# Kernel optimization log

Hardware: AMD Instinct MI355X
Metric: run time of the kernel (lower is better)

## Reference

```python
import jax, jax.numpy as jnp
import numpy as np

V, E, H = 32000, 512, 512
B, S = 64, 128

def setup_inputs() -> dict:
    key = jax.random.key(0)
    ks = jax.random.split(key, 8)
    scale = 1.0 / np.sqrt(H)
    return {
        "decoder_input": jax.random.randint(ks[0], (B, S), 0, V),
        "encoder_hidden": jax.random.normal(ks[1], (1, B, H), dtype=jnp.float32),
        "encoder_output": jax.random.normal(ks[2], (B, S, H), dtype=jnp.float32),
        "emb_table": jax.random.normal(ks[3], (V, E), dtype=jnp.float32),
        "W_ih": jax.random.uniform(ks[4], (3 * H, E), dtype=jnp.float32, minval=-scale, maxval=scale),
        "W_hh": jax.random.uniform(ks[5], (3 * H, H), dtype=jnp.float32, minval=-scale, maxval=scale),
        "b_ih": jax.random.uniform(ks[6], (3 * H,), dtype=jnp.float32, minval=-scale, maxval=scale),
        "b_hh": jax.random.uniform(ks[7], (3 * H,), dtype=jnp.float32, minval=-scale, maxval=scale),
        "epoch": 0,
    }

def _gru_cell(x, h, W_ih, W_hh, b_ih, b_hh):
    # torch GRUCell: gates ordered (r, z, n)
    gi = x @ W_ih.T + b_ih          # [b, 3H]
    gh = h @ W_hh.T + b_hh          # [b, 3H]
    i_r, i_z, i_n = jnp.split(gi, 3, axis=-1)
    h_r, h_z, h_n = jnp.split(gh, 3, axis=-1)
    r = jax.nn.sigmoid(i_r + h_r)
    z = jax.nn.sigmoid(i_z + h_z)
    n = jnp.tanh(i_n + r * h_n)
    return (1.0 - z) * n + z * h

def reference(decoder_input, encoder_hidden, encoder_output, emb_table,
              W_ih, W_hh, b_ih, b_hh, epoch):
    # teacher_force_prob = 1.0 * 0.99**epoch; with epoch=0 teacher forcing always fires,
    # dropout=0 (eval) -> deterministic path.
    embed = emb_table[decoder_input]                 # [b, s, e]
    xs = jnp.transpose(embed, (1, 0, 2))             # [s, b, e] for scan over time
    h0 = encoder_hidden[0]                           # [b, h]

    def step(ht, x_t):
        ht = _gru_cell(x_t, ht, W_ih, W_hh, b_ih, b_hh)              # [b, h]
        scores = jax.nn.softmax(jnp.einsum('bh,bsh->bs', ht, encoder_output), axis=-1)
        context = jnp.einsum('bs,bsh->bh', scores, encoder_output)   # [b, h]
        yt = jnp.concatenate([ht, context], axis=-1)                 # [b, 2h]
        return ht, yt

    _, ys = jax.lax.scan(step, h0, xs)               # ys: [s, b, 2h]
    return jnp.transpose(ys, (1, 0, 2))              # [b, s, 2h]
```

## Files before the change

kernel.cpp:

```cpp
#include <hip/hip_runtime.h>
#include <string.h>

typedef float f32x4 __attribute__((ext_vector_type(4)));

#define B_ 64
#define S_ 128
#define H_ 512
#define NBLK 256
#define GUARD_MAX (1 << 17)


__device__ __forceinline__ int swzW(int k4) { return k4 ^ ((k4 >> 4) & 7); }
__device__ __forceinline__ int swzH(int r, int k4) { return k4 ^ ((r >> 1) & 7); }

__global__ __launch_bounds__(512, 2) void gru_seq(
    const int*   __restrict__ dec,
    const float* __restrict__ eh,
    const float* __restrict__ emb,
    const float* __restrict__ wih,
    const float* __restrict__ whh,
    const float* __restrict__ bih,
    const float* __restrict__ bhh,
    float* __restrict__ out,
    int*   __restrict__ bar)
{
  __shared__ __align__(16) float wih_s[24 * 512];
  __shared__ __align__(16) float whh_s[24 * 512];
  __shared__ __align__(16) float h_s[16 * 512];
  __shared__ float xres[2][16][8][3];
  __shared__ volatile int go;

  const int tid  = threadIdx.x;
  const int wave = tid >> 6;
  const int lane = tid & 63;
  const int bp   = lane & 7;
  const int q    = lane >> 3;
  const int bt   = blockIdx.x >> 6;
  const int ig   = blockIdx.x & 63;
  const int i0   = ig * 8;
  const int b0g  = bt * 16;
  const bool hrole = (wave < 4);
  const int ilA  = (hrole ? wave : (wave - 4)) * 2;
  const int bsel = (q >> 1) & 1, ilsel = q & 1;
  const int my_b  = 2 * bp + bsel;
  const int my_il = ilA + ilsel;
  const int my_i  = i0 + my_il;

  float4* wih4 = (float4*)wih_s;
  float4* whh4 = (float4*)whh_s;
  float4* h4   = (float4*)h_s;

  if (tid == 0) go = 0;

  {
    const int f4 = tid & 127, r0 = tid >> 7;
    #pragma unroll
    for (int m = 0; m < 6; ++m) {
      const int row = r0 + 4 * m;
      const int g = row >> 3, il = row & 7;
      const size_t grow = (size_t)(g * 512 + i0 + il) * 128;
      wih4[row * 128 + swzW(f4)] = ((const float4*)wih)[grow + f4];
      whh4[row * 128 + swzW(f4)] = ((const float4*)whh)[grow + f4];
    }
  }

  float b_ir = 0, b_iz = 0, b_in = 0, b_hr = 0, b_hz = 0, b_hn = 0;
  if (hrole && q < 4) {
    b_ir = bih[my_i]; b_iz = bih[512 + my_i]; b_in = bih[1024 + my_i];
    b_hr = bhh[my_i]; b_hz = bhh[512 + my_i]; b_hn = bhh[1024 + my_i];
  }

  auto xside = [&](int ts) {
    const int tok0 = dec[(b0g + 2 * bp)     * S_ + ts];
    const int tok1 = dec[(b0g + 2 * bp + 1) * S_ + ts];
    const float4* x0 = (const float4*)(emb + (size_t)tok0 * H_);
    const float4* x1 = (const float4*)(emb + (size_t)tok1 * H_);
    const int kq = q * 16;
    float a[2][2][3] = {};
    #pragma unroll 4
    for (int c = 0; c < 16; ++c) {
      const int k4 = kq + c;
      const float4 xv0 = x0[k4];
      const float4 xv1 = x1[k4];
      const int ws = swzW(k4);
      #pragma unroll
      for (int g = 0; g < 3; ++g) {
        #pragma unroll
        for (int e = 0; e < 2; ++e) {
          const float4 wv = wih4[(g * 8 + ilA + e) * 128 + ws];
          a[0][e][g] = fmaf(xv0.x, wv.x, fmaf(xv0.y, wv.y,
                       fmaf(xv0.z, wv.z, fmaf(xv0.w, wv.w, a[0][e][g]))));
          a[1][e][g] = fmaf(xv1.x, wv.x, fmaf(xv1.y, wv.y,
                       fmaf(xv1.z, wv.z, fmaf(xv1.w, wv.w, a[1][e][g]))));
        }
      }
    }
    #pragma unroll
    for (int bb = 0; bb < 2; ++bb)
      #pragma unroll
      for (int e = 0; e < 2; ++e)
        #pragma unroll
        for (int g = 0; g < 3; ++g) {
          float v = a[bb][e][g];
          v += __shfl_xor(v, 8); v += __shfl_xor(v, 16); v += __shfl_xor(v, 32);
          a[bb][e][g] = v;
        }
    if (q < 4) {
      const int buf = ts & 1;
      #pragma unroll
      for (int g = 0; g < 3; ++g)
        xres[buf][my_b][my_il][g] = a[bsel][ilsel][g];
    }
  };

  auto stage_hg = [&](int sh) {
    const int r = tid >> 4, c0 = tid & 15;
    const float* base = out + ((size_t)(b0g + r) * S_ + sh) * 1024 + c0 * 4;
    f32x4 t0, t1, t2, t3, t4, t5, t6, t7;
    asm volatile(
        "global_load_dwordx4 %0, %8, off sc0 sc1\n\t"
        "global_load_dwordx4 %1, %8, off offset:256 sc0 sc1\n\t"
        "global_load_dwordx4 %2, %8, off offset:512 sc0 sc1\n\t"
        "global_load_dwordx4 %3, %8, off offset:768 sc0 sc1\n\t"
        "global_load_dwordx4 %4, %8, off offset:1024 sc0 sc1\n\t"
        "global_load_dwordx4 %5, %8, off offset:1280 sc0 sc1\n\t"
        "global_load_dwordx4 %6, %8, off offset:1536 sc0 sc1\n\t"
        "global_load_dwordx4 %7, %8, off offset:1792 sc0 sc1\n\t"
        "s_waitcnt vmcnt(0)"
        : "=&v"(t0), "=&v"(t1), "=&v"(t2), "=&v"(t3),
          "=&v"(t4), "=&v"(t5), "=&v"(t6), "=&v"(t7)
        : "v"(base) : "memory");
    f32x4* hx = (f32x4*)h_s;
    hx[r * 128 + swzH(r, c0)]       = t0;
    hx[r * 128 + swzH(r, c0 + 16)]  = t1;
    hx[r * 128 + swzH(r, c0 + 32)]  = t2;
    hx[r * 128 + swzH(r, c0 + 48)]  = t3;
    hx[r * 128 + swzH(r, c0 + 64)]  = t4;
    hx[r * 128 + swzH(r, c0 + 80)]  = t5;
    hx[r * 128 + swzH(r, c0 + 96)]  = t6;
    hx[r * 128 + swzH(r, c0 + 112)] = t7;
  };

  __syncthreads();

  if (hrole) {
    const int r = tid >> 4, c0 = tid & 15;
    const float4* src = (const float4*)(eh + (size_t)(b0g + r) * H_);
    #pragma unroll
    for (int j = 0; j < 8; ++j) {
      const int k4 = c0 + 16 * j;
      h4[r * 128 + swzH(r, k4)] = src[k4];
    }
  } else {
    xside(0);
  }
  __syncthreads();

  for (int s = 0; s < S_; ++s) {
    float hnew = 0.f;
    if (hrole) {
      const int kq = q * 16;
      const int br0 = 2 * bp, br1 = br0 + 1;
      float a[2][2][3] = {};
      #pragma unroll 4
      for (int c = 0; c < 16; ++c) {
        const int k4 = kq + c;
        const float4 hv0 = h4[br0 * 128 + swzH(br0, k4)];
        const float4 hv1 = h4[br1 * 128 + swzH(br1, k4)];
        const int ws = swzW(k4);
        #pragma unroll
        for (int g = 0; g < 3; ++g) {
          #pragma unroll
          for (int e = 0; e < 2; ++e) {
            const float4 wv = whh4[(g * 8 + ilA + e) * 128 + ws];
            a[0][e][g] = fmaf(hv0.x, wv.x, fmaf(hv0.y, wv.y,
                         fmaf(hv0.z, wv.z, fmaf(hv0.w, wv.w, a[0][e][g]))));
            a[1][e][g] = fmaf(hv1.x, wv.x, fmaf(hv1.y, wv.y,
                         fmaf(hv1.z, wv.z, fmaf(hv1.w, wv.w, a[1][e][g]))));
          }
        }
      }
      #pragma unroll
      for (int bb = 0; bb < 2; ++bb)
        #pragma unroll
        for (int e = 0; e < 2; ++e)
          #pragma unroll
          for (int g = 0; g < 3; ++g) {
            float v = a[bb][e][g];
            v += __shfl_xor(v, 8); v += __shfl_xor(v, 16); v += __shfl_xor(v, 32);
            a[bb][e][g] = v;
          }
      if (q < 4) {
        const int buf = s & 1;
        const float ir  = xres[buf][my_b][my_il][0] + b_ir;
        const float iz  = xres[buf][my_b][my_il][1] + b_iz;
        const float in2 = xres[buf][my_b][my_il][2] + b_in;
        const float hr = a[bsel][ilsel][0] + b_hr;
        const float hz = a[bsel][ilsel][1] + b_hz;
        const float hn = a[bsel][ilsel][2] + b_hn;
        const float rr = 1.f / (1.f + expf(-(ir + hr)));
        const float zz = 1.f / (1.f + expf(-(iz + hz)));
        const float nn = tanhf(in2 + rr * hn);
        const float hold = h_s[my_b * 512 +
                               (swzH(my_b, my_i >> 2) << 2) + (my_i & 3)];
        hnew = (1.f - zz) * nn + zz * hold;
      }
      const float hpart = __shfl_xor(hnew, 8);
      if (q < 4 && (q & 1) == 0) {
        float2 hv2 = make_float2(hnew, hpart);
        unsigned long long u; memcpy(&u, &hv2, 8);
        __hip_atomic_store(
            (unsigned long long*)(out + ((size_t)(b0g + my_b) * S_ + s) * 1024 + my_i),
            u, __ATOMIC_RELAXED, __HIP_MEMORY_SCOPE_AGENT);
      }
    } else if (s + 1 < S_) {
      xside(s + 1);
    }

    __syncthreads();

    if (s + 1 < S_) {
      if (tid == 0)
        __hip_atomic_store(bar + blockIdx.x, s + 1,
                           __ATOMIC_RELAXED, __HIP_MEMORY_SCOPE_AGENT);
      if (wave == 0) {
        const int* tp = bar + bt * 64 + lane;
        int tk, g2 = 0;
        do {
          asm volatile(
              "global_load_dword %0, %1, off sc0 sc1\n\t"
              "s_waitcnt vmcnt(0)"
              : "=v"(tk) : "v"(tp) : "memory");
        } while (!__all(tk > s) && ++g2 < GUARD_MAX);
        if (lane == 0) go = s + 1;
      } else if (hrole) {
        int g2 = 0;
        while (go < s + 1 && ++g2 < GUARD_MAX) {}
      }
      if (hrole) stage_hg(s);
      __syncthreads();
    }
  }
}

__global__ __launch_bounds__(256) void attn_tiled(
    const float* __restrict__ enc,
    float* __restrict__ out)
{
  __shared__ __align__(16) float enc_s[32 * 512];
  __shared__ __align__(16) float hsm[8 * 512];
  __shared__ float pp[8][128];

  const int tid = threadIdx.x;
  const int b  = blockIdx.x & 63;
  const int sg = blockIdx.x >> 6;
  float4* es4  = (float4*)enc_s;
  float4* hsm4 = (float4*)hsm;

  {
    const int j = tid >> 5, il = tid & 31;
    const float4* hsrc =
        (const float4*)(out + ((size_t)b * S_ + sg * 8 + j) * 1024);
    #pragma unroll
    for (int m = 0; m < 4; ++m) {
      const int k4 = il + 32 * m;
      hsm4[j * 128 + swzW(k4)] = hsrc[k4];
    }
  }
  __syncthreads();

  const int srl = tid >> 3, q8 = tid & 7;
  for (int T = 0; T < 4; ++T) {
    {
      const float4* esrc = (const float4*)(enc + ((size_t)b * S_ + T * 32) * H_);
      #pragma unroll
      for (int m = 0; m < 16; ++m) {
        const int idx = tid + 256 * m;
        const int row = idx >> 7, k4 = idx & 127;
        es4[row * 128 + swzW(k4)] = esrc[row * 128 + k4];
      }
    }
    __syncthreads();
    float acc[8] = {};
    #pragma unroll 4
    for (int c = 0; c < 16; ++c) {
      const int ws = swzW(q8 * 16 + c);
      const float4 ev = es4[srl * 128 + ws];
      #pragma unroll
      for (int j = 0; j < 8; ++j) {
        const float4 hv = hsm4[j * 128 + ws];
        acc[j] = fmaf(ev.x, hv.x, fmaf(ev.y, hv.y,
                 fmaf(ev.z, hv.z, fmaf(ev.w, hv.w, acc[j]))));
      }
    }
    #pragma unroll
    for (int j = 0; j < 8; ++j) {
      acc[j] += __shfl_xor(acc[j], 1);
      acc[j] += __shfl_xor(acc[j], 2);
      acc[j] += __shfl_xor(acc[j], 4);
    }
    if (q8 == 0) {
      #pragma unroll
      for (int j = 0; j < 8; ++j) pp[j][T * 32 + srl] = acc[j];
    }
    __syncthreads();
  }

  {
    const int jg = tid >> 5, l = tid & 31;
    float v0 = pp[jg][l], v1 = pp[jg][l + 32],
          v2 = pp[jg][l + 64], v3 = pp[jg][l + 96];
    float mx = fmaxf(fmaxf(v0, v1), fmaxf(v2, v3));
    #pragma unroll
    for (int o = 16; o > 0; o >>= 1) mx = fmaxf(mx, __shfl_xor(mx, o));
    const float e0 = expf(v0 - mx), e1 = expf(v1 - mx),
                e2 = expf(v2 - mx), e3 = expf(v3 - mx);
    float sm = e0 + e1 + e2 + e3;
    #pragma unroll
    for (int o = 16; o > 0; o >>= 1) sm += __shfl_xor(sm, o);
    const float inv = 1.f / sm;
    pp[jg][l] = e0 * inv; pp[jg][l + 32] = e1 * inv;
    pp[jg][l + 64] = e2 * inv; pp[jg][l + 96] = e3 * inv;
  }
  __syncthreads();

  {
    const int j = tid >> 5, il = tid & 31;
    const float* ecol = enc + (size_t)b * (S_ * H_) + il * 16;
    const float* prow = pp[j];
    float4 c0 = {0,0,0,0}, c1 = {0,0,0,0}, c2 = {0,0,0,0}, c3 = {0,0,0,0};
    #pragma unroll 4
    for (int sr = 0; sr < S_; ++sr) {
      const float p = prow[sr];
      const float4* er = (const float4*)(ecol + (size_t)sr * H_);
      const float4 u0 = er[0], u1 = er[1], u2 = er[2], u3 = er[3];
      c0.x = fmaf(p, u0.x, c0.x); c0.y = fmaf(p, u0.y, c0.y);
      c0.z = fmaf(p, u0.z, c0.z); c0.w = fmaf(p, u0.w, c0.w);
      c1.x = fmaf(p, u1.x, c1.x); c1.y = fmaf(p, u1.y, c1.y);
      c1.z = fmaf(p, u1.z, c1.z); c1.w = fmaf(p, u1.w, c1.w);
      c2.x = fmaf(p, u2.x, c2.x); c2.y = fmaf(p, u2.y, c2.y);
      c2.z = fmaf(p, u2.z, c2.z); c2.w = fmaf(p, u2.w, c2.w);
      c3.x = fmaf(p, u3.x, c3.x); c3.y = fmaf(p, u3.y, c3.y);
      c3.z = fmaf(p, u3.z, c3.z); c3.w = fmaf(p, u3.w, c3.w);
    }
    float4* dst = (float4*)(out + ((size_t)b * S_ + sg * 8 + j) * 1024 +
                            512 + il * 16);
    dst[0] = c0; dst[1] = c1; dst[2] = c2; dst[3] = c3;
  }
}

extern "C" void kernel_launch(void* const* d_in, const int* in_sizes, int n_in,
                              void* d_out, int out_size, void* d_ws, size_t ws_size,
                              hipStream_t stream) {
  (void)in_sizes; (void)n_in; (void)out_size; (void)ws_size;
  const int*   dec = (const int*)d_in[0];
  const float* eh  = (const float*)d_in[1];
  const float* enc = (const float*)d_in[2];
  const float* emb = (const float*)d_in[3];
  const float* wih = (const float*)d_in[4];
  const float* whh = (const float*)d_in[5];
  const float* bih = (const float*)d_in[6];
  const float* bhh = (const float*)d_in[7];
  float* out = (float*)d_out;
  int*   bar = (int*)d_ws;

  hipMemsetAsync(bar, 0, NBLK * sizeof(int), stream);
  gru_seq<<<NBLK, 512, 0, stream>>>(dec, eh, emb, wih, whh, bih, bhh, out, bar);
  attn_tiled<<<16 * B_, 256, 0, stream>>>(enc, out);
}
```

Before: 1.464 ms.

## Hoist input-gate GEMM into separate kernel and retile recurrent GRU blocks

The embedding-times-W_ih projection for all timesteps now runs in a standalone kernel before the recurrence. It writes the r/z pre-activations as fp16 pairs to workspace and stashes the n pre-activation in the context half of the output. The recurrent kernel then keeps only W_hh in shared memory, retiled so each block covers 8 batches × 16 hidden units, and all 8 waves work on the hidden-state matmul. This removes the per-step x-side compute and shrinks the per-step h staging, but adds fp16 rounding of the gate inputs and a separate, non-overlapped precompute pass.

```diff
diff --git a/kernel.cpp b/kernel.cpp
--- a/kernel.cpp
+++ b/kernel.cpp
@@ -1,4 +1,5 @@
 #include <hip/hip_runtime.h>
+#include <hip/hip_fp16.h>
 #include <string.h>
 
 typedef float f32x4 __attribute__((ext_vector_type(4)));
@@ -11,87 +12,180 @@
 
 
 __device__ __forceinline__ int swzW(int k4) { return k4 ^ ((k4 >> 4) & 7); }
-__device__ __forceinline__ int swzH(int r, int k4) { return k4 ^ ((r >> 1) & 7); }
-
-__global__ __launch_bounds__(512, 2) void gru_seq(
+__device__ __forceinline__ int swzH2(int r, int k4) {
+  return k4 ^ ((r >> 1) & 3) ^ (((k4 >> 3) & 1) << 2);
+}
+__device__ __forceinline__ int swzXS(int r, int k4) {
+  return k4 ^ ((k4 >> 3) & 7) ^ ((r >> 1) & 7);
+}
+
+__global__ __launch_bounds__(512, 2) void xgemm(
     const int*   __restrict__ dec,
-    const float* __restrict__ eh,
     const float* __restrict__ emb,
     const float* __restrict__ wih,
+    const float* __restrict__ bih,
+    float* __restrict__ out,
+    unsigned int* __restrict__ xgrz)
+{
+  __shared__ __align__(16) float xs[32 * 512];
+  f32x4* xs4 = (f32x4*)xs;
+  const int tid = threadIdx.x;
+  const int b  = blockIdx.x >> 2;
+  const int sg = blockIdx.x & 3;
+
+  {
+    const int r = tid >> 4, c = tid & 15;
+    const int tok = dec[b * S_ + sg * 32 + r];
+    const f32x4* src = (const f32x4*)(emb + (size_t)tok * H_);
+    #pragma unroll
+    for (int m = 0; m < 8; ++m) {
+      const int k4 = m * 16 + c;
+      xs4[r * 128 + swzXS(r, k4)] = src[k4];
+    }
+  }
+  __syncthreads();
+
+  const int lane = tid & 63, wave = tid >> 6;
+  const int bp = lane & 7, q = lane >> 3;
+  const int kq = q * 16;
+  const int r0 = 2 * bp, r1 = r0 + 1, r2 = 16 + r0, r3 = r2 + 1;
+  const float4* w4 = (const float4*)wih;
+
+  for (int og = wave * 32; og < wave * 32 + 32; ++og) {
+    float a[4][2][3] = {};
+    #pragma unroll 4
+    for (int c = 0; c < 16; ++c) {
+      const int k4 = kq + c;
+      const f32x4 x0 = xs4[r0 * 128 + swzXS(r0, k4)];
+      const f32x4 x1 = xs4[r1 * 128 + swzXS(r1, k4)];
+      const f32x4 x2 = xs4[r2 * 128 + swzXS(r2, k4)];
+      const f32x4 x3 = xs4[r3 * 128 + swzXS(r3, k4)];
+      #pragma unroll
+      for (int g = 0; g < 3; ++g) {
+        #pragma unroll
+        for (int e = 0; e < 2; ++e) {
+          const float4 wv = w4[(size_t)(g * 512 + og * 2 + e) * 128 + k4];
+          a[0][e][g] = fmaf(x0.x, wv.x, fmaf(x0.y, wv.y,
+                       fmaf(x0.z, wv.z, fmaf(x0.w, wv.w, a[0][e][g]))));
+          a[1][e][g] = fmaf(x1.x, wv.x, fmaf(x1.y, wv.y,
+                       fmaf(x1.z, wv.z, fmaf(x1.w, wv.w, a[1][e][g]))));
+          a[2][e][g] = fmaf(x2.x, wv.x, fmaf(x2.y, wv.y,
+                       fmaf(x2.z, wv.z, fmaf(x2.w, wv.w, a[2][e][g]))));
+          a[3][e][g] = fmaf(x3.x, wv.x, fmaf(x3.y, wv.y,
+                       fmaf(x3.z, wv.z, fmaf(x3.w, wv.w, a[3][e][g]))));
+        }
+      }
+    }
+    #pragma unroll
+    for (int t = 0; t < 4; ++t)
+      #pragma unroll
+      for (int e = 0; e < 2; ++e)
+        #pragma unroll
+        for (int g = 0; g < 3; ++g) {
+          float v = a[t][e][g];
+          v += __shfl_xor(v, 8); v += __shfl_xor(v, 16); v += __shfl_xor(v, 32);
+          a[t][e][g] = v;
+        }
+    {
+      const int tk = q >> 1, e = q & 1;
+      const int sl = (tk >> 1) * 16 + 2 * bp + (tk & 1);
+      const int i  = og * 2 + e;
+      const float ar = a[tk][e][0] + bih[i];
+      const float az = a[tk][e][1] + bih[512 + i];
+      const float an = a[tk][e][2] + bih[1024 + i];
+      __half2 h2; h2.x = __float2half(ar); h2.y = __float2half(az);
+      const size_t tb = (size_t)b * S_ + sg * 32 + sl;
+      unsigned int u; memcpy(&u, &h2, 4);
+      xgrz[tb * 512 + i] = u;
+      out[tb * 1024 + 512 + i] = an;
+    }
+  }
+}
+
+__global__ __launch_bounds__(512, 2) void gru_seq(
+    const float* __restrict__ eh,
     const float* __restrict__ whh,
-    const float* __restrict__ bih,
     const float* __restrict__ bhh,
     float* __restrict__ out,
-    int*   __restrict__ bar)
+    const unsigned int* __restrict__ xgrz,
+    int* __restrict__ bar)
 {
-  __shared__ __align__(16) float wih_s[24 * 512];
-  __shared__ __align__(16) float whh_s[24 * 512];
-  __shared__ __align__(16) float h_s[16 * 512];
-  __shared__ float xres[2][16][8][3];
-  __shared__ volatile int go;
+  __shared__ __align__(16) float whh_s[48 * 512];
+  __shared__ __align__(16) float h_s[8 * 512];
+  __shared__ int go_w;
+  volatile int* gop = &go_w;
 
   const int tid  = threadIdx.x;
   const int wave = tid >> 6;
   const int lane = tid & 63;
-  const int bp   = lane & 7;
-  const int q    = lane >> 3;
-  const int bt   = blockIdx.x >> 6;
-  const int ig   = blockIdx.x & 63;
-  const int i0   = ig * 8;
-  const int b0g  = bt * 16;
-  const bool hrole = (wave < 4);
-  const int ilA  = (hrole ? wave : (wave - 4)) * 2;
+  const int bp   = lane & 3;
+  const int q    = lane >> 2;
+  const int bt   = blockIdx.x >> 5;
+  const int ig   = blockIdx.x & 31;
+  const int i0   = ig * 16;
+  const int b0g  = bt * 8;
+  const int ilA  = 2 * wave;
   const int bsel = (q >> 1) & 1, ilsel = q & 1;
   const int my_b  = 2 * bp + bsel;
   const int my_il = ilA + ilsel;
   const int my_i  = i0 + my_il;
 
-  float4* wih4 = (float4*)wih_s;
-  float4* whh4 = (float4*)whh_s;
-  float4* h4   = (float4*)h_s;
-
-  if (tid == 0) go = 0;
-
-  {
-    const int f4 = tid & 127, r0 = tid >> 7;
-    #pragma unroll
-    for (int m = 0; m < 6; ++m) {
-      const int row = r0 + 4 * m;
-      const int g = row >> 3, il = row & 7;
-      const size_t grow = (size_t)(g * 512 + i0 + il) * 128;
-      wih4[row * 128 + swzW(f4)] = ((const float4*)wih)[grow + f4];
-      whh4[row * 128 + swzW(f4)] = ((const float4*)whh)[grow + f4];
-    }
-  }
-
-  float b_ir = 0, b_iz = 0, b_in = 0, b_hr = 0, b_hz = 0, b_hn = 0;
-  if (hrole && q < 4) {
-    b_ir = bih[my_i]; b_iz = bih[512 + my_i]; b_in = bih[1024 + my_i];
+  f32x4* whh4 = (f32x4*)whh_s;
+  f32x4* h4   = (f32x4*)h_s;
+
+  if (tid == 0) *gop = 0;
+
+  {
+    const int f4 = tid & 127, rb = tid >> 7;
+    #pragma unroll
+    for (int m = 0; m < 12; ++m) {
+      const int lr = rb + 4 * m;
+      const int g = lr >> 4, il = lr & 15;
+      whh4[lr * 128 + swzW(f4)] =
+          ((const f32x4*)whh)[(size_t)(g * 512 + i0 + il) * 128 + f4];
+    }
+  }
+
+  float b_hr = 0, b_hz = 0, b_hn = 0;
+  if (q < 4) {
     b_hr = bhh[my_i]; b_hz = bhh[512 + my_i]; b_hn = bhh[1024 + my_i];
   }
 
-  auto xside = [&](int ts) {
-    const int tok0 = dec[(b0g + 2 * bp)     * S_ + ts];
-    const int tok1 = dec[(b0g + 2 * bp + 1) * S_ + ts];
-    const float4* x0 = (const float4*)(emb + (size_t)tok0 * H_);
-    const float4* x1 = (const float4*)(emb + (size_t)tok1 * H_);
-    const int kq = q * 16;
+  {
+    const int r = tid >> 6, c0 = tid & 63;
+    const f32x4* src = (const f32x4*)(eh + (size_t)(b0g + r) * H_);
+    h4[r * 128 + swzH2(r, c0)]      = src[c0];
+    h4[r * 128 + swzH2(r, c0 + 64)] = src[c0 + 64];
+  }
+  __syncthreads();
+
+  const int br0 = 2 * bp, br1 = br0 + 1;
+  const int kq = q * 8;
+
+  for (int s = 0; s < S_; ++s) {
+    float xn_v = 0.f; unsigned int rz_v = 0;
+    if (q < 4) {
+      const size_t tb = (size_t)(b0g + my_b) * S_ + s;
+      xn_v = out[tb * 1024 + 512 + my_i];
+      rz_v = xgrz[tb * 512 + my_i];
+    }
+
     float a[2][2][3] = {};
-    #pragma unroll 4
-    for (int c = 0; c < 16; ++c) {
+    #pragma unroll
+    for (int c = 0; c < 8; ++c) {
       const int k4 = kq + c;
-      const float4 xv0 = x0[k4];
-      const float4 xv1 = x1[k4];
+      const f32x4 hv0 = h4[br0 * 128 + swzH2(br0, k4)];
+      const f32x4 hv1 = h4[br1 * 128 + swzH2(br1, k4)];
       const int ws = swzW(k4);
       #pragma unroll
       for (int g = 0; g < 3; ++g) {
         #pragma unroll
         for (int e = 0; e < 2; ++e) {
-          const float4 wv = wih4[(g * 8 + ilA + e) * 128 + ws];
-          a[0][e][g] = fmaf(xv0.x, wv.x, fmaf(xv0.y, wv.y,
-                       fmaf(xv0.z, wv.z, fmaf(xv0.w, wv.w, a[0][e][g]))));
-          a[1][e][g] = fmaf(xv1.x, wv.x, fmaf(xv1.y, wv.y,
-                       fmaf(xv1.z, wv.z, fmaf(xv1.w, wv.w, a[1][e][g]))));
+          const f32x4 wv = whh4[(g * 16 + ilA + e) * 128 + ws];
+          a[0][e][g] = fmaf(hv0.x, wv.x, fmaf(hv0.y, wv.y,
+                       fmaf(hv0.z, wv.z, fmaf(hv0.w, wv.w, a[0][e][g]))));
+          a[1][e][g] = fmaf(hv1.x, wv.x, fmaf(hv1.y, wv.y,
+                       fmaf(hv1.z, wv.z, fmaf(hv1.w, wv.w, a[1][e][g]))));
         }
       }
     }
@@ -102,144 +196,70 @@
         #pragma unroll
         for (int g = 0; g < 3; ++g) {
           float v = a[bb][e][g];
-          v += __shfl_xor(v, 8); v += __shfl_xor(v, 16); v += __shfl_xor(v, 32);
+          v += __shfl_xor(v, 4);  v += __shfl_xor(v, 8);
+          v += __shfl_xor(v, 16); v += __shfl_xor(v, 32);
           a[bb][e][g] = v;
         }
+
     if (q < 4) {
-      const int buf = ts & 1;
-      #pragma unroll
-      for (int g = 0; g < 3; ++g)
-        xres[buf][my_b][my_il][g] = a[bsel][ilsel][g];
-    }
-  };
-
-  auto stage_hg = [&](int sh) {
-    const int r = tid >> 4, c0 = tid & 15;
-    const float* base = out + ((size_t)(b0g + r) * S_ + sh) * 1024 + c0 * 4;
-    f32x4 t0, t1, t2, t3, t4, t5, t6, t7;
-    asm volatile(
-        "global_load_dwordx4 %0, %8, off sc0 sc1\n\t"
-        "global_load_dwordx4 %1, %8, off offset:256 sc0 sc1\n\t"
-        "global_load_dwordx4 %2, %8, off offset:512 sc0 sc1\n\t"
-        "global_load_dwordx4 %3, %8, off offset:768 sc0 sc1\n\t"
-        "global_load_dwordx4 %4, %8, off offset:1024 sc0 sc1\n\t"
-        "global_load_dwordx4 %5, %8, off offset:1280 sc0 sc1\n\t"
-        "global_load_dwordx4 %6, %8, off offset:1536 sc0 sc1\n\t"
-        "global_load_dwordx4 %7, %8, off offset:1792 sc0 sc1\n\t"
-        "s_waitcnt vmcnt(0)"
-        : "=&v"(t0), "=&v"(t1), "=&v"(t2), "=&v"(t3),
-          "=&v"(t4), "=&v"(t5), "=&v"(t6), "=&v"(t7)
-        : "v"(base) : "memory");
-    f32x4* hx = (f32x4*)h_s;
-    hx[r * 128 + swzH(r, c0)]       = t0;
-    hx[r * 128 + swzH(r, c0 + 16)]  = t1;
-    hx[r * 128 + swzH(r, c0 + 32)]  = t2;
-    hx[r * 128 + swzH(r, c0 + 48)]  = t3;
-    hx[r * 128 + swzH(r, c0 + 64)]  = t4;
-    hx[r * 128 + swzH(r, c0 + 80)]  = t5;
-    hx[r * 128 + swzH(r, c0 + 96)]  = t6;
-    hx[r * 128 + swzH(r, c0 + 112)] = t7;
-  };
-
-  __syncthreads();
-
-  if (hrole) {
-    const int r = tid >> 4, c0 = tid & 15;
-    const float4* src = (const float4*)(eh + (size_t)(b0g + r) * H_);
-    #pragma unroll
-    for (int j = 0; j < 8; ++j) {
-      const int k4 = c0 + 16 * j;
-      h4[r * 128 + swzH(r, k4)] = src[k4];
-    }
-  } else {
-    xside(0);
-  }
-  __syncthreads();
-
-  for (int s = 0; s < S_; ++s) {
-    float hnew = 0.f;
-    if (hrole) {
-      const int kq = q * 16;
-      const int br0 = 2 * bp, br1 = br0 + 1;
-      float a[2][2][3] = {};
-      #pragma unroll 4
-      for (int c = 0; c < 16; ++c) {
-        const int k4 = kq + c;
-        const float4 hv0 = h4[br0 * 128 + swzH(br0, k4)];
-        const float4 hv1 = h4[br1 * 128 + swzH(br1, k4)];
-        const int ws = swzW(k4);
-        #pragma unroll
-        for (int g = 0; g < 3; ++g) {
-          #pragma unroll
-          for (int e = 0; e < 2; ++e) {
-            const float4 wv = whh4[(g * 8 + ilA + e) * 128 + ws];
-            a[0][e][g] = fmaf(hv0.x, wv.x, fmaf(hv0.y, wv.y,
-                         fmaf(hv0.z, wv.z, fmaf(hv0.w, wv.w, a[0][e][g]))));
-            a[1][e][g] = fmaf(hv1.x, wv.x, fmaf(hv1.y, wv.y,
-                         fmaf(hv1.z, wv.z, fmaf(hv1.w, wv.w, a[1][e][g]))));
-          }
-        }
-      }
-      #pragma unroll
-      for (int bb = 0; bb < 2; ++bb)
-        #pragma unroll
-        for (int e = 0; e < 2; ++e)
-          #pragma unroll
-          for (int g = 0; g < 3; ++g) {
-            float v = a[bb][e][g];
-            v += __shfl_xor(v, 8); v += __shfl_xor(v, 16); v += __shfl_xor(v, 32);
-            a[bb][e][g] = v;
-          }
-      if (q < 4) {
-        const int buf = s & 1;
-        const float ir  = xres[buf][my_b][my_il][0] + b_ir;
-        const float iz  = xres[buf][my_b][my_il][1] + b_iz;
-        const float in2 = xres[buf][my_b][my_il][2] + b_in;
-        const float hr = a[bsel][ilsel][0] + b_hr;
-        const float hz = a[bsel][ilsel][1] + b_hz;
-        const float hn = a[bsel][ilsel][2] + b_hn;
-        const float rr = 1.f / (1.f + expf(-(ir + hr)));
-        const float zz = 1.f / (1.f + expf(-(iz + hz)));
-        const float nn = tanhf(in2 + rr * hn);
-        const float hold = h_s[my_b * 512 +
-                               (swzH(my_b, my_i >> 2) << 2) + (my_i & 3)];
-        hnew = (1.f - zz) * nn + zz * hold;
-      }
-      const float hpart = __shfl_xor(hnew, 8);
-      if (q < 4 && (q & 1) == 0) {
+      __half2 rz; memcpy(&rz, &rz_v, 4);
+      const float ir  = __half2float(rz.x);
+      const float iz  = __half2float(rz.y);
+      const float hr = a[bsel][ilsel][0] + b_hr;
+      const float hz = a[bsel][ilsel][1] + b_hz;
+      const float hn = a[bsel][ilsel][2] + b_hn;
+      const float rr = 1.f / (1.f + expf(-(ir + hr)));
+      const float zz = 1.f / (1.f + expf(-(iz + hz)));
+      const float nn = tanhf(xn_v + rr * hn);
+      const int f4a = my_b * 128 + swzH2(my_b, my_i >> 2);
+      const float hold = h_s[f4a * 4 + (my_i & 3)];
+      const float hnew = (1.f - zz) * nn + zz * hold;
+      const float hpart = __shfl_xor(hnew, 4);
+      if ((q & 1) == 0) {
         float2 hv2 = make_float2(hnew, hpart);
         unsigned long long u; memcpy(&u, &hv2, 8);
         __hip_atomic_store(
-            (unsigned long long*)(out + ((size_t)(b0g + my_b) * S_ + s) * 1024 + my_i),
+            (unsigned long long*)(out + ((size_t)(b0g + my_b) * S_ + s) * 1024
+                                  + i0 + ilA),
             u, __ATOMIC_RELAXED, __HIP_MEMORY_SCOPE_AGENT);
       }
-    } else if (s + 1 < S_) {
-      xside(s + 1);
     }
 
     __syncthreads();
-
-    if (s + 1 < S_) {
-      if (tid == 0)
-        __hip_atomic_store(bar + blockIdx.x, s + 1,
-                           __ATOMIC_RELAXED, __HIP_MEMORY_SCOPE_AGENT);
-      if (wave == 0) {
-        const int* tp = bar + bt * 64 + lane;
-        int tk, g2 = 0;
-        do {
-          asm volatile(
-              "global_load_dword %0, %1, off sc0 sc1\n\t"
-              "s_waitcnt vmcnt(0)"
-              : "=v"(tk) : "v"(tp) : "memory");
-        } while (!__all(tk > s) && ++g2 < GUARD_MAX);
-        if (lane == 0) go = s + 1;
-      } else if (hrole) {
-        int g2 = 0;
-        while (go < s + 1 && ++g2 < GUARD_MAX) {}
-      }
-      if (hrole) stage_hg(s);
-      __syncthreads();
-    }
+    if (s + 1 == S_) break;
+
+    if (tid == 0)
+      __hip_atomic_store(bar + blockIdx.x, s + 1,
+                         __ATOMIC_RELAXED, __HIP_MEMORY_SCOPE_AGENT);
+    if (wave == 0) {
+      const int* tp = bar + bt * 32 + (lane & 31);
+      int tk, g2 = 0;
+      do {
+        asm volatile(
+            "global_load_dword %0, %1, off sc0 sc1\n\t"
+            "s_waitcnt vmcnt(0)"
+            : "=v"(tk) : "v"(tp) : "memory");
+      } while (!__all(tk > s) && ++g2 < GUARD_MAX);
+      if (lane == 0) *gop = s + 1;
+    } else {
+      int g2 = 0;
+      while (*gop < s + 1 && ++g2 < GUARD_MAX) {}
+    }
+    __builtin_amdgcn_sched_barrier(0);
+
+    {
+      const int r = tid >> 6, c0 = tid & 63;
+      const float* base = out + ((size_t)(b0g + r) * S_ + s) * 1024 + c0 * 4;
+      f32x4 t0, t1;
+      asm volatile(
+          "global_load_dwordx4 %0, %2, off sc0 sc1\n\t"
+          "global_load_dwordx4 %1, %2, off offset:1024 sc0 sc1\n\t"
+          "s_waitcnt vmcnt(0)"
+          : "=&v"(t0), "=&v"(t1) : "v"(base) : "memory");
+      h4[r * 128 + swzH2(r, c0)]      = t0;
+      h4[r * 128 + swzH2(r, c0 + 64)] = t1;
+    }
+    __syncthreads();
   }
 }
 
@@ -362,9 +382,11 @@
   const float* bih = (const float*)d_in[6];
   const float* bhh = (const float*)d_in[7];
   float* out = (float*)d_out;
-  int*   bar = (int*)d_ws;
+  unsigned int* xgrz = (unsigned int*)d_ws;
+  int* bar = (int*)((char*)d_ws + (16u << 20));
 
   hipMemsetAsync(bar, 0, NBLK * sizeof(int), stream);
-  gru_seq<<<NBLK, 512, 0, stream>>>(dec, eh, emb, wih, whh, bih, bhh, out, bar);
+  xgemm<<<NBLK, 512, 0, stream>>>(dec, emb, wih, bih, out, xgrz);
+  gru_seq<<<NBLK, 512, 0, stream>>>(eh, whh, bhh, out, xgrz, bar);
   attn_tiled<<<16 * B_, 256, 0, stream>>>(enc, out);
 }
```

Measured after the change: 1.514 ms. 1.03x slower.
